# Performance work log

Measured on AMD Instinct MI355X. Metric: run time of the kernel, lower is better.

Reference implementation:

```python
import jax, jax.numpy as jnp
import numpy as np

NUM_FIELDS = 40
# upper-triangular (i<j) field pair indices, computed once at trace time
_I_IDX, _J_IDX = np.triu_indices(NUM_FIELDS, k=1)  # each length 780


def setup_inputs() -> dict:
    key = jax.random.key(0)
    k1, k2 = jax.random.split(key)
    batch, num_fields, embed_dim = 8192, NUM_FIELDS, 32
    num_interactions = num_fields * (num_fields - 1) // 2  # 780
    embeddings = jax.random.normal(k1, (batch, num_fields, embed_dim), dtype=jnp.float32)
    W = jax.random.normal(k2, (num_interactions, embed_dim, embed_dim), dtype=jnp.float32)
    return {"embeddings": embeddings, "W": W}


def reference(embeddings, W):
    # embeddings: (b, f, e); W: (k, e, e) with k = f*(f-1)/2
    vi = embeddings[:, _I_IDX, :]  # (b, k, e)
    vj = embeddings[:, _J_IDX, :]  # (b, k, e)
    # per-pair bilinear form, reduced over embed dims -> (b, k)
    return jnp.einsum('bke,kef,bkf->bk', vi, W, vj)
```

## Files before the change

### kernel.cpp

```cpp
#include <hip/hip_runtime.h>
#include <cstdint>
#include <cstddef>

typedef __attribute__((ext_vector_type(8))) short short8;
typedef __attribute__((ext_vector_type(4))) unsigned short ushort4_t;
typedef __attribute__((ext_vector_type(4))) float f32x4;

#define NF 40
#define NK 780
#define BT 32
#define THREADS 1024

__device__ __forceinline__ unsigned short f2bf(float f) {
    unsigned int u = __float_as_uint(f);
    u = (u + 0x7fffu + ((u >> 16) & 1u)) >> 16;
    return (unsigned short)u;
}
__device__ __forceinline__ float bf2f(unsigned short x) {
    return __uint_as_float(((unsigned int)x) << 16);
}

__global__ __launch_bounds__(128) void wprep_kernel(const float* __restrict__ W,
                                                    unsigned short* __restrict__ wfrag) {
    const int k = blockIdx.x, t = threadIdx.x;
    const int half = t >> 6, l = t & 63;
    const int e = (l & 15) + 16 * half;
    const int f0 = 8 * (l >> 4);
    const float* src = W + (size_t)k * 1024 + e * 32 + f0;
    const float4 x0 = *(const float4*)src;
    const float4 x1 = *(const float4*)(src + 4);
    short8 v;
    v[0] = (short)f2bf(x0.x); v[1] = (short)f2bf(x0.y);
    v[2] = (short)f2bf(x0.z); v[3] = (short)f2bf(x0.w);
    v[4] = (short)f2bf(x1.x); v[5] = (short)f2bf(x1.y);
    v[6] = (short)f2bf(x1.z); v[7] = (short)f2bf(x1.w);
    *(short8*)(wfrag + (size_t)k * 1024 + half * 512 + l * 8) = v;
}


#define RELOAD_VI()                                                                     \
    {                                                                                   \
        const int i7 = ii & 7;                                                          \
        const char* ibase = embT + (ii << 11) + eoff;                                   \
        const ushort4_t ra = *(const ushort4_t*)(ibase + (((bq      + fqlo32) ^ i7) << 4)); \
        const ushort4_t rb = *(const ushort4_t*)(ibase + (((bq + 64 + fqlo32) ^ i7) << 4)); \
        const ushort4_t rc = *(const ushort4_t*)(ibase + (((bq + 16 + fqlo32) ^ i7) << 4)); \
        const ushort4_t rd = *(const ushort4_t*)(ibase + (((bq + 80 + fqlo32) ^ i7) << 4)); \
        vf00 = bf2f(ra[0]); vf01 = bf2f(ra[1]); vf02 = bf2f(ra[2]); vf03 = bf2f(ra[3]); \
        vf04 = bf2f(rb[0]); vf05 = bf2f(rb[1]); vf06 = bf2f(rb[2]); vf07 = bf2f(rb[3]); \
        vf10 = bf2f(rc[0]); vf11 = bf2f(rc[1]); vf12 = bf2f(rc[2]); vf13 = bf2f(rc[3]); \
        vf14 = bf2f(rd[0]); vf15 = bf2f(rd[1]); vf16 = bf2f(rd[2]); vf17 = bf2f(rd[3]); \
    }

#define KSTEP(AE0, AE1, OREG)                                                           \
    {                                                                                   \
        const int j7 = jj & 7;                                                          \
        const char* jbase = embT + (jj << 11);                                          \
        const short8 vj0 = *(const short8*)(jbase + (((bq      + fq32) ^ j7) << 4));    \
        const short8 vj1 = *(const short8*)(jbase + (((bq + 16 + fq32) ^ j7) << 4));    \
        f32x4 t00 = {}, t01 = {}, t10 = {}, t11 = {};                                   \
        t00 = __builtin_amdgcn_mfma_f32_16x16x32_bf16(AE0, vj0, t00, 0, 0, 0);          \
        t10 = __builtin_amdgcn_mfma_f32_16x16x32_bf16(AE1, vj0, t10, 0, 0, 0);          \
        t01 = __builtin_amdgcn_mfma_f32_16x16x32_bf16(AE0, vj1, t01, 0, 0, 0);          \
        t11 = __builtin_amdgcn_mfma_f32_16x16x32_bf16(AE1, vj1, t11, 0, 0, 0);          \
        float p0 = t00[0]*vf00 + t00[1]*vf01 + t00[2]*vf02 + t00[3]*vf03                \
                 + t10[0]*vf04 + t10[1]*vf05 + t10[2]*vf06 + t10[3]*vf07;               \
        float p1 = t01[0]*vf10 + t01[1]*vf11 + t01[2]*vf12 + t01[3]*vf13                \
                 + t11[0]*vf14 + t11[1]*vf15 + t11[2]*vf16 + t11[3]*vf17;               \
        p0 += __shfl_xor(p0, 16); p0 += __shfl_xor(p0, 32);                             \
        p1 += __shfl_xor(p1, 16); p1 += __shfl_xor(p1, 32);                             \
        OREG = (l & 16) ? p1 : p0;                                                      \
        ++jj;                                                                           \
        if (jj == NF) { ++ii; jj = ii + 1; RELOAD_VI(); }                               \
    }

__global__ __launch_bounds__(THREADS, 4) void bil_kernel(const float* __restrict__ emb,
                                                         const unsigned short* __restrict__ wfrag,
                                                         float* __restrict__ out) {
    __shared__ __align__(16) char embT[NF * 2048];

    const int tid = threadIdx.x;
    const int b0 = blockIdx.x * BT;

    for (int u = tid; u < BT * 160; u += THREADS) {
        const int bb = u / 160;
        const int t = u - 160 * bb;
        const int field = t >> 2;
        const int fq = t & 3;
        const float* src = emb + (size_t)(b0 + bb) * (NF * 32) + field * 32 + 8 * fq;
        const float4 x0 = *(const float4*)src;
        const float4 x1 = *(const float4*)(src + 4);
        short8 v;
        v[0] = (short)f2bf(x0.x); v[1] = (short)f2bf(x0.y);
        v[2] = (short)f2bf(x0.z); v[3] = (short)f2bf(x0.w);
        v[4] = (short)f2bf(x1.x); v[5] = (short)f2bf(x1.y);
        v[6] = (short)f2bf(x1.z); v[7] = (short)f2bf(x1.w);
        const int g = (bb + 32 * fq) ^ (field & 7);
        *(short8*)(embT + field * 2048 + g * 16) = v;
    }
    __syncthreads();

    const int ww = tid >> 6;
    const int l = tid & 63;
    const int bq = l & 15;
    const int h = l >> 4;
    const int fq32 = h << 5;
    const int fqlo32 = (h >> 1) << 5;
    const int eoff = (h & 1) * 8;

    const int ps = 2 * ((195 * ww) >> 4);
    const int pe = 2 * ((195 * (ww + 1)) >> 4);

    int ii = 0, jj;
    {
        int kk = 2 * ps, len = 39;
        while (kk >= len) { kk -= len; ++ii; --len; }
        jj = ii + 1 + kk;
    }

    float vf00, vf01, vf02, vf03, vf04, vf05, vf06, vf07;
    float vf10, vf11, vf12, vf13, vf14, vf15, vf16, vf17;
    RELOAD_VI();

    const short8* wf = (const short8*)wfrag;

    size_t gb = (size_t)(2 * ps) * 128;
    short8 c0e0 = wf[gb + l],       c0e1 = wf[gb + 64 + l];
    short8 c1e0 = wf[gb + 128 + l], c1e1 = wf[gb + 192 + l];
    short8 c2e0 = wf[gb + 256 + l], c2e1 = wf[gb + 320 + l];
    short8 c3e0 = wf[gb + 384 + l], c3e1 = wf[gb + 448 + l];

    for (int pg = ps; pg < pe; pg += 2) {
        const bool more = (pg + 2) < pe;
        short8 n0e0 = {}, n0e1 = {}, n1e0 = {}, n1e1 = {};
        short8 n2e0 = {}, n2e1 = {}, n3e0 = {}, n3e1 = {};
        if (more) {
            const size_t nb = (size_t)(2 * (pg + 2)) * 128;
            n0e0 = wf[nb + l];       n0e1 = wf[nb + 64 + l];
            n1e0 = wf[nb + 128 + l]; n1e1 = wf[nb + 192 + l];
            n2e0 = wf[nb + 256 + l]; n2e1 = wf[nb + 320 + l];
            n3e0 = wf[nb + 384 + l]; n3e1 = wf[nb + 448 + l];
        }
        float o0, o1, o2, o3;
        KSTEP(c0e0, c0e1, o0);
        KSTEP(c1e0, c1e1, o1);
        KSTEP(c2e0, c2e1, o2);
        KSTEP(c3e0, c3e1, o3);
        if (l < 32) {
            float4 st; st.x = o0; st.y = o1; st.z = o2; st.w = o3;
            *(float4*)(out + (size_t)(b0 + l) * NK + 2 * pg) = st;
        }
        if (more) {
            c0e0 = n0e0; c0e1 = n0e1; c1e0 = n1e0; c1e1 = n1e1;
            c2e0 = n2e0; c2e1 = n2e1; c3e0 = n3e0; c3e1 = n3e1;
        }
    }
}

extern "C" void kernel_launch(void* const* d_in, const int* in_sizes, int n_in,
                              void* d_out, int out_size, void* d_ws, size_t ws_size,
                              hipStream_t stream) {
    const float* emb = (const float*)d_in[0];
    const float* W   = (const float*)d_in[1];
    float* out = (float*)d_out;
    unsigned short* wfrag = (unsigned short*)d_ws;

    wprep_kernel<<<dim3(NK), dim3(128), 0, stream>>>(W, wfrag);
    bil_kernel<<<dim3(8192 / BT), dim3(THREADS), 0, stream>>>(emb, wfrag, out);
}
```

Baseline: 44.04 us.

## Switch pair contraction to 32x32x16 MFMA with ping-pong W prefetch

```diff
diff --git a/kernel.cpp b/kernel.cpp
--- a/kernel.cpp
+++ b/kernel.cpp
@@ -4,7 +4,7 @@
 
 typedef __attribute__((ext_vector_type(8))) short short8;
 typedef __attribute__((ext_vector_type(4))) unsigned short ushort4_t;
-typedef __attribute__((ext_vector_type(4))) float f32x4;
+typedef __attribute__((ext_vector_type(16))) float f32x16;
 
 #define NF 40
 #define NK 780
@@ -24,8 +24,8 @@
                                                     unsigned short* __restrict__ wfrag) {
     const int k = blockIdx.x, t = threadIdx.x;
     const int half = t >> 6, l = t & 63;
-    const int e = (l & 15) + 16 * half;
-    const int f0 = 8 * (l >> 4);
+    const int e = l & 31;
+    const int f0 = 16 * half + 8 * (l >> 5);
     const float* src = W + (size_t)k * 1024 + e * 32 + f0;
     const float4 x0 = *(const float4*)src;
     const float4 x1 = *(const float4*)(src + 4);
@@ -42,41 +42,46 @@
     {                                                                                   \
         const int i7 = ii & 7;                                                          \
         const char* ibase = embT + (ii << 11) + eoff;                                   \
-        const ushort4_t ra = *(const ushort4_t*)(ibase + (((bq      + fqlo32) ^ i7) << 4)); \
-        const ushort4_t rb = *(const ushort4_t*)(ibase + (((bq + 64 + fqlo32) ^ i7) << 4)); \
-        const ushort4_t rc = *(const ushort4_t*)(ibase + (((bq + 16 + fqlo32) ^ i7) << 4)); \
-        const ushort4_t rd = *(const ushort4_t*)(ibase + (((bq + 80 + fqlo32) ^ i7) << 4)); \
-        vf00 = bf2f(ra[0]); vf01 = bf2f(ra[1]); vf02 = bf2f(ra[2]); vf03 = bf2f(ra[3]); \
-        vf04 = bf2f(rb[0]); vf05 = bf2f(rb[1]); vf06 = bf2f(rb[2]); vf07 = bf2f(rb[3]); \
-        vf10 = bf2f(rc[0]); vf11 = bf2f(rc[1]); vf12 = bf2f(rc[2]); vf13 = bf2f(rc[3]); \
-        vf14 = bf2f(rd[0]); vf15 = bf2f(rd[1]); vf16 = bf2f(rd[2]); vf17 = bf2f(rd[3]); \
+        const ushort4_t r0 = *(const ushort4_t*)(ibase + (((b32     ) ^ i7) << 4));     \
+        const ushort4_t r1 = *(const ushort4_t*)(ibase + (((b32 + 32) ^ i7) << 4));     \
+        const ushort4_t r2 = *(const ushort4_t*)(ibase + (((b32 + 64) ^ i7) << 4));     \
+        const ushort4_t r3 = *(const ushort4_t*)(ibase + (((b32 + 96) ^ i7) << 4));     \
+        vf0  = bf2f(r0[0]); vf1  = bf2f(r0[1]); vf2  = bf2f(r0[2]); vf3  = bf2f(r0[3]); \
+        vf4  = bf2f(r1[0]); vf5  = bf2f(r1[1]); vf6  = bf2f(r1[2]); vf7  = bf2f(r1[3]); \
+        vf8  = bf2f(r2[0]); vf9  = bf2f(r2[1]); vf10 = bf2f(r2[2]); vf11 = bf2f(r2[3]); \
+        vf12 = bf2f(r3[0]); vf13 = bf2f(r3[1]); vf14 = bf2f(r3[2]); vf15 = bf2f(r3[3]); \
     }
 
-#define KSTEP(AE0, AE1, OREG)                                                           \
+#define KSTEP(A0, A1, OREG)                                                             \
     {                                                                                   \
         const int j7 = jj & 7;                                                          \
         const char* jbase = embT + (jj << 11);                                          \
-        const short8 vj0 = *(const short8*)(jbase + (((bq      + fq32) ^ j7) << 4));    \
-        const short8 vj1 = *(const short8*)(jbase + (((bq + 16 + fq32) ^ j7) << 4));    \
-        f32x4 t00 = {}, t01 = {}, t10 = {}, t11 = {};                                   \
-        t00 = __builtin_amdgcn_mfma_f32_16x16x32_bf16(AE0, vj0, t00, 0, 0, 0);          \
-        t10 = __builtin_amdgcn_mfma_f32_16x16x32_bf16(AE1, vj0, t10, 0, 0, 0);          \
-        t01 = __builtin_amdgcn_mfma_f32_16x16x32_bf16(AE0, vj1, t01, 0, 0, 0);          \
-        t11 = __builtin_amdgcn_mfma_f32_16x16x32_bf16(AE1, vj1, t11, 0, 0, 0);          \
-        float p0 = t00[0]*vf00 + t00[1]*vf01 + t00[2]*vf02 + t00[3]*vf03                \
-                 + t10[0]*vf04 + t10[1]*vf05 + t10[2]*vf06 + t10[3]*vf07;               \
-        float p1 = t01[0]*vf10 + t01[1]*vf11 + t01[2]*vf12 + t01[3]*vf13                \
-                 + t11[0]*vf14 + t11[1]*vf15 + t11[2]*vf16 + t11[3]*vf17;               \
-        p0 += __shfl_xor(p0, 16); p0 += __shfl_xor(p0, 32);                             \
-        p1 += __shfl_xor(p1, 16); p1 += __shfl_xor(p1, 32);                             \
-        OREG = (l & 16) ? p1 : p0;                                                      \
+        const short8 vj0 = *(const short8*)(jbase + (((b32 + fq0) ^ j7) << 4));         \
+        const short8 vj1 = *(const short8*)(jbase + (((b32 + fq1) ^ j7) << 4));         \
+        f32x16 t = {};                                                                  \
+        t = __builtin_amdgcn_mfma_f32_32x32x16_bf16(A0, vj0, t, 0, 0, 0);               \
+        t = __builtin_amdgcn_mfma_f32_32x32x16_bf16(A1, vj1, t, 0, 0, 0);               \
+        float p = t[0]*vf0  + t[1]*vf1  + t[2]*vf2   + t[3]*vf3                         \
+                + t[4]*vf4  + t[5]*vf5  + t[6]*vf6   + t[7]*vf7                         \
+                + t[8]*vf8  + t[9]*vf9  + t[10]*vf10 + t[11]*vf11                       \
+                + t[12]*vf12+ t[13]*vf13+ t[14]*vf14 + t[15]*vf15;                      \
+        p += __shfl_xor(p, 32);                                                         \
+        OREG = p;                                                                       \
         ++jj;                                                                           \
         if (jj == NF) { ++ii; jj = ii + 1; RELOAD_VI(); }                               \
     }
 
-__global__ __launch_bounds__(THREADS, 4) void bil_kernel(const float* __restrict__ emb,
-                                                         const unsigned short* __restrict__ wfrag,
-                                                         float* __restrict__ out) {
+#define LOADW2(R0, R1, R2, R3, KB)                                                      \
+    {                                                                                   \
+        const int kbc = (KB) > 778 ? 778 : (KB);                                        \
+        const size_t bs = (size_t)kbc << 7;                                             \
+        R0 = wf[bs + l];       R1 = wf[bs + 64 + l];                                    \
+        R2 = wf[bs + 128 + l]; R3 = wf[bs + 192 + l];                                   \
+    }
+
+__global__ __launch_bounds__(THREADS) void bil_kernel(const float* __restrict__ emb,
+                                                      const unsigned short* __restrict__ wfrag,
+                                                      float* __restrict__ out) {
     __shared__ __align__(16) char embT[NF * 2048];
 
     const int tid = threadIdx.x;
@@ -102,57 +107,60 @@
 
     const int ww = tid >> 6;
     const int l = tid & 63;
-    const int bq = l & 15;
-    const int h = l >> 4;
-    const int fq32 = h << 5;
-    const int fqlo32 = (h >> 1) << 5;
-    const int eoff = (h & 1) * 8;
+    const int b32 = l & 31;
+    const int h32 = l >> 5;
+    const int fq0 = 32 * h32;
+    const int fq1 = 64 + 32 * h32;
+    const int eoff = 8 * h32;
 
-    const int ps = 2 * ((195 * ww) >> 4);
-    const int pe = 2 * ((195 * (ww + 1)) >> 4);
+    const int ks = 4 * ((195 * ww) >> 4);
+    const int ke = 4 * ((195 * (ww + 1)) >> 4);
 
     int ii = 0, jj;
     {
-        int kk = 2 * ps, len = 39;
+        int kk = ks, len = 39;
         while (kk >= len) { kk -= len; ++ii; --len; }
         jj = ii + 1 + kk;
     }
 
-    float vf00, vf01, vf02, vf03, vf04, vf05, vf06, vf07;
-    float vf10, vf11, vf12, vf13, vf14, vf15, vf16, vf17;
+    float vf0, vf1, vf2, vf3, vf4, vf5, vf6, vf7;
+    float vf8, vf9, vf10, vf11, vf12, vf13, vf14, vf15;
     RELOAD_VI();
 
     const short8* wf = (const short8*)wfrag;
 
-    size_t gb = (size_t)(2 * ps) * 128;
-    short8 c0e0 = wf[gb + l],       c0e1 = wf[gb + 64 + l];
-    short8 c1e0 = wf[gb + 128 + l], c1e1 = wf[gb + 192 + l];
-    short8 c2e0 = wf[gb + 256 + l], c2e1 = wf[gb + 320 + l];
-    short8 c3e0 = wf[gb + 384 + l], c3e1 = wf[gb + 448 + l];
+    short8 a0, a1, a2, a3;
+    short8 bb0, bb1, bb2, bb3;
+    LOADW2(a0, a1, a2, a3, ks);
 
-    for (int pg = ps; pg < pe; pg += 2) {
-        const bool more = (pg + 2) < pe;
-        short8 n0e0 = {}, n0e1 = {}, n1e0 = {}, n1e1 = {};
-        short8 n2e0 = {}, n2e1 = {}, n3e0 = {}, n3e1 = {};
-        if (more) {
-            const size_t nb = (size_t)(2 * (pg + 2)) * 128;
-            n0e0 = wf[nb + l];       n0e1 = wf[nb + 64 + l];
-            n1e0 = wf[nb + 128 + l]; n1e1 = wf[nb + 192 + l];
-            n2e0 = wf[nb + 256 + l]; n2e1 = wf[nb + 320 + l];
-            n3e0 = wf[nb + 384 + l]; n3e1 = wf[nb + 448 + l];
+    int kcur = ks;
+    while (kcur + 8 <= ke) {
+        float o0, o1, o2, o3, o4, o5, o6, o7;
+        LOADW2(bb0, bb1, bb2, bb3, kcur + 2);
+        KSTEP(a0, a1, o0);  KSTEP(a2, a3, o1);
+        LOADW2(a0, a1, a2, a3, kcur + 4);
+        KSTEP(bb0, bb1, o2); KSTEP(bb2, bb3, o3);
+        LOADW2(bb0, bb1, bb2, bb3, kcur + 6);
+        KSTEP(a0, a1, o4);  KSTEP(a2, a3, o5);
+        LOADW2(a0, a1, a2, a3, kcur + 8);
+        KSTEP(bb0, bb1, o6); KSTEP(bb2, bb3, o7);
+        if (l < 32) {
+            float* orow = out + (size_t)(b0 + l) * NK + kcur;
+            float4 s0; s0.x = o0; s0.y = o1; s0.z = o2; s0.w = o3;
+            float4 s1; s1.x = o4; s1.y = o5; s1.z = o6; s1.w = o7;
+            *(float4*)orow = s0;
+            *(float4*)(orow + 4) = s1;
         }
+        kcur += 8;
+    }
+    if (kcur < ke) {
         float o0, o1, o2, o3;
-        KSTEP(c0e0, c0e1, o0);
-        KSTEP(c1e0, c1e1, o1);
-        KSTEP(c2e0, c2e1, o2);
-        KSTEP(c3e0, c3e1, o3);
+        LOADW2(bb0, bb1, bb2, bb3, kcur + 2);
+        KSTEP(a0, a1, o0);  KSTEP(a2, a3, o1);
+        KSTEP(bb0, bb1, o2); KSTEP(bb2, bb3, o3);
         if (l < 32) {
-            float4 st; st.x = o0; st.y = o1; st.z = o2; st.w = o3;
-            *(float4*)(out + (size_t)(b0 + l) * NK + 2 * pg) = st;
-        }
-        if (more) {
-            c0e0 = n0e0; c0e1 = n0e1; c1e0 = n1e0; c1e1 = n1e1;
-            c2e0 = n2e0; c2e1 = n2e1; c3e0 = n3e0; c3e1 = n3e1;
+            float4 s0; s0.x = o0; s0.y = o1; s0.z = o2; s0.w = o3;
+            *(float4*)(out + (size_t)(b0 + l) * NK + kcur) = s0;
         }
     }
 }
```

After: 41.33 us. -6.2%, faster.
